# Kernel optimization log

Hardware: AMD Instinct MI355X
Metric: run time of the kernel (lower is better)

Reference implementation:

```python
import jax, jax.numpy as jnp
import numpy as np

TEMPERATURE = 0.1
B, T, D = 8, 1024, 1024
NEG_INF = -1e30

def setup_inputs() -> dict:
    key = jax.random.key(0)
    k1, k2, k3 = jax.random.split(key, 3)
    features = jax.random.normal(k1, (B, T, D), dtype=jnp.float32)
    masks = jax.random.bernoulli(k2, 0.05, (B, 1, T, T)).astype(jnp.float32)
    input_coords_length = jax.random.randint(k3, (B,), T // 2, T - 1)  # int32
    return {"features": features, "masks": masks, "input_coords_length": input_coords_length}


def _sup_con_loss(feat, mask, L):
    # feat: [T, D], mask: [T, T] float, L: scalar int valid length (slice [:L, :L])
    Tn = feat.shape[0]
    dt = feat.dtype
    vr = jnp.arange(Tn) < L                              # valid rows/cols [T]
    valid2d = (vr[:, None] & vr[None, :]).astype(dt)     # [T, T]
    dot = jnp.matmul(feat, feat.T) / TEMPERATURE         # [T, T]
    dot = jnp.where(vr[None, :], dot, NEG_INF)           # exclude padded cols from max
    logits = dot - jax.lax.stop_gradient(jnp.max(dot, axis=-1, keepdims=True))
    logits_mask = (1.0 - jnp.eye(Tn, dtype=dt)) * valid2d  # off-diagonal, in-slice
    exp_logits = jnp.exp(logits) * logits_mask
    m = mask * valid2d
    # negative_mask = 1-mask; entries < 1 zeroed (binary mask -> indicator of mask==0)
    neg = 1.0 - m
    neg = jnp.where(neg < 1.0, 0.0, neg) * valid2d
    # positive_mask = mask with entries > 0 set to 1
    pos = jnp.where(m > 0, 1.0, m)
    neg_denom = jnp.sum(exp_logits * neg, axis=-1, keepdims=True)
    pos_denom = jax.lax.stop_gradient(jnp.sum(exp_logits * pos, axis=-1, keepdims=True))
    log_prob = logits - jnp.log(neg_denom + pos_denom + 1e-6)
    m2 = m * logits_mask
    mean_log_prob_pos = (m2 * log_prob).sum(-1) / (m2.sum(-1) + 1e-6)  # [T]
    # mean over the L valid rows only (matches .mean() on the sliced tensor)
    return -jnp.sum(jnp.where(vr, mean_log_prob_pos, 0.0)) / L.astype(dt)


def _is_valid(mask, L):
    # valid sample iff sliced mask differs from eye(L) with [0,0]=0
    Tn = mask.shape[0]
    vr = jnp.arange(Tn) < L
    valid2d = (vr[:, None] & vr[None, :]).astype(mask.dtype)
    sanity = jnp.eye(Tn, dtype=mask.dtype).at[0, 0].set(0.0) * valid2d
    return jnp.any((mask * valid2d) != sanity)


def reference(features, masks, input_coords_length):
    L = input_coords_length + 1                      # [B]
    mask0 = masks[:, 0]                              # [B, T, T] (num_layers asserted == 1)
    losses = jax.vmap(_sup_con_loss)(features, mask0, L)   # [B]
    valid = jax.vmap(_is_valid)(mask0, L)                  # [B] bool
    vbs = jnp.maximum(jnp.sum(valid.astype(features.dtype)), 1.0)
    return jnp.sum(losses) / vbs
```

## Files before the change

kernel.cpp:

```cpp
#include <hip/hip_runtime.h>
#include <hip/hip_bf16.h>
#include <stdint.h>

#define T_DIM 1024
#define B_DIM 8

typedef __attribute__((ext_vector_type(8))) short short8;
typedef __attribute__((ext_vector_type(4))) float f32x4;

__device__ inline void gll16(const void* g, void* l) {
  __builtin_amdgcn_global_load_lds((__attribute__((address_space(1))) void*)g,
                                   (__attribute__((address_space(3))) void*)l,
                                   16, 0, 0);
}

__global__ __launch_bounds__(256) void convert_kernel(const float* __restrict__ F,
                                                      __hip_bfloat16* __restrict__ Fb) {
  const int t = blockIdx.x * 256 + threadIdx.x;
  const float4 v = ((const float4*)F)[t];
  union { __hip_bfloat16 h[4]; uint64_t u; } p;
  p.h[0] = __float2bfloat16(v.x);
  p.h[1] = __float2bfloat16(v.y);
  p.h[2] = __float2bfloat16(v.z);
  p.h[3] = __float2bfloat16(v.w);
  ((uint64_t*)Fb)[t] = p.u;
}

__global__ __launch_bounds__(512) void fused_kernel(const __hip_bfloat16* __restrict__ Fb,
                                                    const float* __restrict__ M,
                                                    const int* __restrict__ icl,
                                                    float* __restrict__ part) {
  const int b  = blockIdx.z;
  const int rt = blockIdx.y;
  const int ct = blockIdx.x;
  const int L  = icl[b] + 1;
  if (rt * 128 >= L || ct * 128 >= L) return;

  __shared__ char smem[65536];
  __hip_bfloat16* As = (__hip_bfloat16*)smem;
  __hip_bfloat16* Bs = (__hip_bfloat16*)(smem + 32768);
  float* rp = (float*)smem;
  float* rp_m = rp;
  float* rp_d = rp + 512;
  float* rp_s = rp + 1024;
  float* rp_c = rp + 1536;
  float* rp_b = rp + 2048;

  const __hip_bfloat16* F = Fb + ((size_t)b << 20);
  const int tid  = threadIdx.x;
  const int lane = tid & 63;
  const int wave = tid >> 6;
  const int wrow = (wave >> 2) * 64;
  const int wcol = (wave & 3) * 32;
  const int row0 = rt * 128;
  const int col0 = ct * 128;
  const bool diag = (rt == ct);

  const int fr = lane & 15;
  const int q  = lane >> 4;
  const int sl8 = (q ^ ((fr >> 1) & 3)) * 8;

  const int srow = tid >> 2;
  const int sgk  = (((tid & 3) ^ ((tid >> 3) & 3)) * 8);

  f32x4 acc[4][2];
#pragma unroll
  for (int i = 0; i < 4; i++)
#pragma unroll
    for (int j = 0; j < 2; j++) acc[i][j] = (f32x4){0.f, 0.f, 0.f, 0.f};

  for (int k0 = 0; k0 < T_DIM; k0 += 128) {
    __syncthreads();
#pragma unroll
    for (int p = 0; p < 4; p++)
      gll16(F + (size_t)(row0 + srow) * T_DIM + k0 + p * 32 + sgk,
            As + p * 4096 + tid * 8);
    if (!diag) {
#pragma unroll
      for (int p = 0; p < 4; p++)
        gll16(F + (size_t)(col0 + srow) * T_DIM + k0 + p * 32 + sgk,
              Bs + p * 4096 + tid * 8);
    }
    __syncthreads();
#pragma unroll
    for (int kk = 0; kk < 4; kk++) {
      const __hip_bfloat16* Ab = As + kk * 4096;
      const __hip_bfloat16* Bb = diag ? Ab : (Bs + kk * 4096);
      short8 af[4], bfr[2];
#pragma unroll
      for (int t = 0; t < 4; t++)
        af[t] = *(const short8*)(Ab + (wrow + t * 16 + fr) * 32 + sl8);
#pragma unroll
      for (int j = 0; j < 2; j++)
        bfr[j] = *(const short8*)(Bb + (wcol + j * 16 + fr) * 32 + sl8);
#pragma unroll
      for (int ti = 0; ti < 4; ti++)
#pragma unroll
        for (int tj = 0; tj < 2; tj++)
          acc[ti][tj] = __builtin_amdgcn_mfma_f32_16x16x32_bf16(af[ti], bfr[tj], acc[ti][tj], 0, 0, 0);
    }
  }
  __syncthreads();

  const float* Mb = M + ((size_t)b << 20);
  const int gc0 = col0 + wcol + fr;
  const int gc1 = gc0 + 16;
#pragma unroll
  for (int ti = 0; ti < 4; ti++) {
    float mk0[4], mk1[4];
#pragma unroll
    for (int r = 0; r < 4; r++) {
      const int grow = row0 + wrow + ti * 16 + q * 4 + r;
      mk0[r] = (gc0 < L) ? Mb[(size_t)grow * T_DIM + gc0] : 0.f;
      mk1[r] = (gc1 < L) ? Mb[(size_t)grow * T_DIM + gc1] : 0.f;
    }
#pragma unroll
    for (int r = 0; r < 4; r++) {
      const int lrow = wrow + ti * 16 + q * 4 + r;
      const int grow = row0 + lrow;
      const float s0 = (gc0 < L) ? acc[ti][0][r] * 10.0f : -1e30f;
      const float s1 = (gc1 < L) ? acc[ti][1][r] * 10.0f : -1e30f;
      float m = fmaxf(s0, s1);
#pragma unroll
      for (int d = 1; d < 16; d <<= 1) m = fmaxf(m, __shfl_xor(m, d, 64));
      float den = 0.f, msum = 0.f, cnt = 0.f, badf = 0.f;
      if (gc0 < L) {
        if (gc0 != grow) { den += __expf(s0 - m); msum += mk0[r] * s0; cnt += mk0[r]; }
        const float sane = (gc0 == grow && grow != 0) ? 1.f : 0.f;
        badf = fmaxf(badf, (mk0[r] != sane) ? 1.f : 0.f);
      }
      if (gc1 < L) {
        if (gc1 != grow) { den += __expf(s1 - m); msum += mk1[r] * s1; cnt += mk1[r]; }
        const float sane = (gc1 == grow && grow != 0) ? 1.f : 0.f;
        badf = fmaxf(badf, (mk1[r] != sane) ? 1.f : 0.f);
      }
#pragma unroll
      for (int d = 1; d < 16; d <<= 1) {
        den  += __shfl_xor(den, d, 64);
        msum += __shfl_xor(msum, d, 64);
        cnt  += __shfl_xor(cnt, d, 64);
        badf  = fmaxf(badf, __shfl_xor(badf, d, 64));
      }
      if (fr == 0) {
        const int slot = wave & 3;
        rp_m[lrow * 4 + slot] = m;   rp_d[lrow * 4 + slot] = den;
        rp_s[lrow * 4 + slot] = msum; rp_c[lrow * 4 + slot] = cnt;
        rp_b[lrow * 4 + slot] = badf;
      }
    }
  }
  __syncthreads();

  if (tid < 128) {
    float m = -1e30f;
#pragma unroll
    for (int s = 0; s < 4; s++) m = fmaxf(m, rp_m[tid * 4 + s]);
    float den = 0.f, msum = 0.f, cnt = 0.f, badf = 0.f;
#pragma unroll
    for (int s = 0; s < 4; s++) {
      den  += rp_d[tid * 4 + s] * __expf(rp_m[tid * 4 + s] - m);
      msum += rp_s[tid * 4 + s];
      cnt  += rp_c[tid * 4 + s];
      badf  = fmaxf(badf, rp_b[tid * 4 + s]);
    }
    float* p = part + ((((size_t)b * 1024 + row0 + tid) * 8) + ct) * 5;
    p[0] = m; p[1] = den; p[2] = msum; p[3] = cnt; p[4] = badf;
  }
}

__global__ __launch_bounds__(256) void reduce_kernel(const float* __restrict__ part,
                                                     const int* __restrict__ icl,
                                                     float* __restrict__ blk_sum,
                                                     int* __restrict__ blk_bad) {
  const int blk = blockIdx.x;
  const int row = blk * 256 + threadIdx.x;
  const int b = row >> 10;
  const int i = row & 1023;
  const int L = icl[b] + 1;
  float rv = 0.f;
  int bad = 0;
  if (i < L) {
    const float* p = part + (size_t)row * 40;
    const int ns = (L + 127) >> 7;
    float m = -1e30f;
    for (int s = 0; s < ns; s++) m = fmaxf(m, p[s * 5 + 0]);
    float den = 0.f, msum = 0.f, cnt = 0.f, badf = 0.f;
    for (int s = 0; s < ns; s++) {
      den  += p[s * 5 + 1] * __expf(p[s * 5 + 0] - m);
      msum += p[s * 5 + 2];
      cnt  += p[s * 5 + 3];
      badf  = fmaxf(badf, p[s * 5 + 4]);
    }
    const float A = msum - cnt * m;
    const float mlpp = (A - cnt * __logf(den + 1e-6f)) / (cnt + 1e-6f);
    rv = -mlpp / (float)L;
    bad = badf > 0.f ? 1 : 0;
  }
  const int tid  = threadIdx.x;
  const int lane = tid & 63;
  const int wave = tid >> 6;
  for (int o = 32; o > 0; o >>= 1) rv += __shfl_down(rv, o, 64);
  const int wbad = (__ballot(bad) != 0ull) ? 1 : 0;
  __shared__ float sred[4];
  __shared__ int bred[4];
  if (lane == 0) { sred[wave] = rv; bred[wave] = wbad; }
  __syncthreads();
  if (tid == 0) {
    blk_sum[blk] = sred[0] + sred[1] + sred[2] + sred[3];
    blk_bad[blk] = bred[0] | bred[1] | bred[2] | bred[3];
  }
}

__global__ __launch_bounds__(64) void final_kernel(const float* __restrict__ blk_sum,
                                                   const int* __restrict__ blk_bad,
                                                   float* __restrict__ out) {
  const int tid = threadIdx.x;
  float v = (tid < 32) ? blk_sum[tid] : 0.f;
  for (int o = 32; o > 0; o >>= 1) v += __shfl_down(v, o, 64);
  if (tid == 0) {
    int vcount = 0;
    for (int bb = 0; bb < B_DIM; bb++) {
      const int any = blk_bad[bb * 4] | blk_bad[bb * 4 + 1] |
                      blk_bad[bb * 4 + 2] | blk_bad[bb * 4 + 3];
      vcount += any ? 1 : 0;
    }
    out[0] = v / fmaxf((float)vcount, 1.0f);
  }
}

extern "C" void kernel_launch(void* const* d_in, const int* in_sizes, int n_in,
                              void* d_out, int out_size, void* d_ws, size_t ws_size,
                              hipStream_t stream) {
  const float* feat = (const float*)d_in[0];
  const float* mask = (const float*)d_in[1];
  const int*   icl  = (const int*)d_in[2];
  float* out = (float*)d_out;

  char* ws = (char*)d_ws;
  __hip_bfloat16* Fb = (__hip_bfloat16*)ws;
  float* part    = (float*)(ws + (16u << 20));
  float* blk_sum = (float*)(ws + (18u << 20));
  int*   blk_bad = (int*)(ws + (18u << 20) + 512);

  convert_kernel<<<dim3(8192), dim3(256), 0, stream>>>(feat, Fb);
  fused_kernel<<<dim3(8, 8, 8), dim3(512), 0, stream>>>(Fb, mask, icl, part);
  reduce_kernel<<<dim3(32), dim3(256), 0, stream>>>(part, icl, blk_sum, blk_bad);
  final_kernel<<<dim3(1), dim3(64), 0, stream>>>(blk_sum, blk_bad, out);
}
```

Baseline: 134.0 us.

## Shrink GEMM tiles to 64x64 and fold final reduction into last reduce block

The fused GEMM+loss kernel now uses 64x64 output tiles with 256 threads and a 64-wide K step, giving a 16x16x8 grid. The aim is more blocks and higher occupancy, since the 128-tile grid left many CUs idle once tiles past L are skipped. The separate final kernel is removed: reduce blocks publish their partials with release stores and bump an atomic counter, and the last block computes the output. The counter is reset inside the convert kernel. The cost is more redundant global and L2 traffic per tile, twice as many partial slots to reduce, and a dependence on atomic ordering across kernels.

```diff
diff --git a/kernel.cpp b/kernel.cpp
--- a/kernel.cpp
+++ b/kernel.cpp
@@ -15,8 +15,10 @@
 }
 
 __global__ __launch_bounds__(256) void convert_kernel(const float* __restrict__ F,
-                                                      __hip_bfloat16* __restrict__ Fb) {
+                                                      __hip_bfloat16* __restrict__ Fb,
+                                                      int* __restrict__ counter) {
   const int t = blockIdx.x * 256 + threadIdx.x;
+  if (t == 0) __hip_atomic_store(counter, 0, __ATOMIC_RELAXED, __HIP_MEMORY_SCOPE_AGENT);
   const float4 v = ((const float4*)F)[t];
   union { __hip_bfloat16 h[4]; uint64_t u; } p;
   p.h[0] = __float2bfloat16(v.x);
@@ -26,34 +28,34 @@
   ((uint64_t*)Fb)[t] = p.u;
 }
 
-__global__ __launch_bounds__(512) void fused_kernel(const __hip_bfloat16* __restrict__ Fb,
-                                                    const float* __restrict__ M,
-                                                    const int* __restrict__ icl,
-                                                    float* __restrict__ part) {
+__global__ __launch_bounds__(256, 6) void fused_kernel(const __hip_bfloat16* __restrict__ Fb,
+                                                       const float* __restrict__ M,
+                                                       const int* __restrict__ icl,
+                                                       float* __restrict__ part) {
   const int b  = blockIdx.z;
   const int rt = blockIdx.y;
   const int ct = blockIdx.x;
   const int L  = icl[b] + 1;
-  if (rt * 128 >= L || ct * 128 >= L) return;
-
-  __shared__ char smem[65536];
+  if (rt * 64 >= L || ct * 64 >= L) return;
+
+  __shared__ char smem[16384];
   __hip_bfloat16* As = (__hip_bfloat16*)smem;
-  __hip_bfloat16* Bs = (__hip_bfloat16*)(smem + 32768);
+  __hip_bfloat16* Bs = (__hip_bfloat16*)(smem + 8192);
   float* rp = (float*)smem;
   float* rp_m = rp;
-  float* rp_d = rp + 512;
-  float* rp_s = rp + 1024;
-  float* rp_c = rp + 1536;
-  float* rp_b = rp + 2048;
+  float* rp_d = rp + 128;
+  float* rp_s = rp + 256;
+  float* rp_c = rp + 384;
+  float* rp_b = rp + 512;
 
   const __hip_bfloat16* F = Fb + ((size_t)b << 20);
   const int tid  = threadIdx.x;
   const int lane = tid & 63;
   const int wave = tid >> 6;
-  const int wrow = (wave >> 2) * 64;
-  const int wcol = (wave & 3) * 32;
-  const int row0 = rt * 128;
-  const int col0 = ct * 128;
+  const int wrow = (wave >> 1) * 32;
+  const int wcol = (wave & 1) * 32;
+  const int row0 = rt * 64;
+  const int col0 = ct * 64;
   const bool diag = (rt == ct);
 
   const int fr = lane & 15;
@@ -63,38 +65,34 @@
   const int srow = tid >> 2;
   const int sgk  = (((tid & 3) ^ ((tid >> 3) & 3)) * 8);
 
-  f32x4 acc[4][2];
-#pragma unroll
-  for (int i = 0; i < 4; i++)
+  f32x4 acc[2][2];
+#pragma unroll
+  for (int i = 0; i < 2; i++)
 #pragma unroll
     for (int j = 0; j < 2; j++) acc[i][j] = (f32x4){0.f, 0.f, 0.f, 0.f};
 
-  for (int k0 = 0; k0 < T_DIM; k0 += 128) {
+  for (int k0 = 0; k0 < T_DIM; k0 += 64) {
     __syncthreads();
-#pragma unroll
-    for (int p = 0; p < 4; p++)
-      gll16(F + (size_t)(row0 + srow) * T_DIM + k0 + p * 32 + sgk,
-            As + p * 4096 + tid * 8);
+    gll16(F + (size_t)(row0 + srow) * T_DIM + k0 + sgk,      As + tid * 8);
+    gll16(F + (size_t)(row0 + srow) * T_DIM + k0 + 32 + sgk, As + 2048 + tid * 8);
     if (!diag) {
-#pragma unroll
-      for (int p = 0; p < 4; p++)
-        gll16(F + (size_t)(col0 + srow) * T_DIM + k0 + p * 32 + sgk,
-              Bs + p * 4096 + tid * 8);
+      gll16(F + (size_t)(col0 + srow) * T_DIM + k0 + sgk,      Bs + tid * 8);
+      gll16(F + (size_t)(col0 + srow) * T_DIM + k0 + 32 + sgk, Bs + 2048 + tid * 8);
     }
     __syncthreads();
 #pragma unroll
-    for (int kk = 0; kk < 4; kk++) {
-      const __hip_bfloat16* Ab = As + kk * 4096;
-      const __hip_bfloat16* Bb = diag ? Ab : (Bs + kk * 4096);
-      short8 af[4], bfr[2];
-#pragma unroll
-      for (int t = 0; t < 4; t++)
+    for (int kk = 0; kk < 2; kk++) {
+      const __hip_bfloat16* Ab = As + kk * 2048;
+      const __hip_bfloat16* Bb = diag ? Ab : (Bs + kk * 2048);
+      short8 af[2], bfr[2];
+#pragma unroll
+      for (int t = 0; t < 2; t++)
         af[t] = *(const short8*)(Ab + (wrow + t * 16 + fr) * 32 + sl8);
 #pragma unroll
       for (int j = 0; j < 2; j++)
         bfr[j] = *(const short8*)(Bb + (wcol + j * 16 + fr) * 32 + sl8);
 #pragma unroll
-      for (int ti = 0; ti < 4; ti++)
+      for (int ti = 0; ti < 2; ti++)
 #pragma unroll
         for (int tj = 0; tj < 2; tj++)
           acc[ti][tj] = __builtin_amdgcn_mfma_f32_16x16x32_bf16(af[ti], bfr[tj], acc[ti][tj], 0, 0, 0);
@@ -106,7 +104,7 @@
   const int gc0 = col0 + wcol + fr;
   const int gc1 = gc0 + 16;
 #pragma unroll
-  for (int ti = 0; ti < 4; ti++) {
+  for (int ti = 0; ti < 2; ti++) {
     float mk0[4], mk1[4];
 #pragma unroll
     for (int r = 0; r < 4; r++) {
@@ -142,28 +140,24 @@
         badf  = fmaxf(badf, __shfl_xor(badf, d, 64));
       }
       if (fr == 0) {
-        const int slot = wave & 3;
-        rp_m[lrow * 4 + slot] = m;   rp_d[lrow * 4 + slot] = den;
-        rp_s[lrow * 4 + slot] = msum; rp_c[lrow * 4 + slot] = cnt;
-        rp_b[lrow * 4 + slot] = badf;
+        const int slot = wave & 1;
+        rp_m[lrow * 2 + slot] = m;    rp_d[lrow * 2 + slot] = den;
+        rp_s[lrow * 2 + slot] = msum; rp_c[lrow * 2 + slot] = cnt;
+        rp_b[lrow * 2 + slot] = badf;
       }
     }
   }
   __syncthreads();
 
-  if (tid < 128) {
-    float m = -1e30f;
-#pragma unroll
-    for (int s = 0; s < 4; s++) m = fmaxf(m, rp_m[tid * 4 + s]);
-    float den = 0.f, msum = 0.f, cnt = 0.f, badf = 0.f;
-#pragma unroll
-    for (int s = 0; s < 4; s++) {
-      den  += rp_d[tid * 4 + s] * __expf(rp_m[tid * 4 + s] - m);
-      msum += rp_s[tid * 4 + s];
-      cnt  += rp_c[tid * 4 + s];
-      badf  = fmaxf(badf, rp_b[tid * 4 + s]);
-    }
-    float* p = part + ((((size_t)b * 1024 + row0 + tid) * 8) + ct) * 5;
+  if (tid < 64) {
+    const float m0 = rp_m[tid * 2 + 0], m1 = rp_m[tid * 2 + 1];
+    const float m = fmaxf(m0, m1);
+    const float den = rp_d[tid * 2 + 0] * __expf(m0 - m) +
+                      rp_d[tid * 2 + 1] * __expf(m1 - m);
+    const float msum = rp_s[tid * 2 + 0] + rp_s[tid * 2 + 1];
+    const float cnt  = rp_c[tid * 2 + 0] + rp_c[tid * 2 + 1];
+    const float badf = fmaxf(rp_b[tid * 2 + 0], rp_b[tid * 2 + 1]);
+    float* p = part + ((((size_t)b * 1024 + row0 + tid) * 16) + ct) * 5;
     p[0] = m; p[1] = den; p[2] = msum; p[3] = cnt; p[4] = badf;
   }
 }
@@ -171,7 +165,9 @@
 __global__ __launch_bounds__(256) void reduce_kernel(const float* __restrict__ part,
                                                      const int* __restrict__ icl,
                                                      float* __restrict__ blk_sum,
-                                                     int* __restrict__ blk_bad) {
+                                                     int* __restrict__ blk_bad,
+                                                     int* __restrict__ counter,
+                                                     float* __restrict__ out) {
   const int blk = blockIdx.x;
   const int row = blk * 256 + threadIdx.x;
   const int b = row >> 10;
@@ -180,8 +176,8 @@
   float rv = 0.f;
   int bad = 0;
   if (i < L) {
-    const float* p = part + (size_t)row * 40;
-    const int ns = (L + 127) >> 7;
+    const float* p = part + (size_t)row * 80;
+    const int ns = (L + 63) >> 6;
     float m = -1e30f;
     for (int s = 0; s < ns; s++) m = fmaxf(m, p[s * 5 + 0]);
     float den = 0.f, msum = 0.f, cnt = 0.f, badf = 0.f;
@@ -206,25 +202,24 @@
   if (lane == 0) { sred[wave] = rv; bred[wave] = wbad; }
   __syncthreads();
   if (tid == 0) {
-    blk_sum[blk] = sred[0] + sred[1] + sred[2] + sred[3];
-    blk_bad[blk] = bred[0] | bred[1] | bred[2] | bred[3];
-  }
-}
-
-__global__ __launch_bounds__(64) void final_kernel(const float* __restrict__ blk_sum,
-                                                   const int* __restrict__ blk_bad,
-                                                   float* __restrict__ out) {
-  const int tid = threadIdx.x;
-  float v = (tid < 32) ? blk_sum[tid] : 0.f;
-  for (int o = 32; o > 0; o >>= 1) v += __shfl_down(v, o, 64);
-  if (tid == 0) {
-    int vcount = 0;
-    for (int bb = 0; bb < B_DIM; bb++) {
-      const int any = blk_bad[bb * 4] | blk_bad[bb * 4 + 1] |
-                      blk_bad[bb * 4 + 2] | blk_bad[bb * 4 + 3];
-      vcount += any ? 1 : 0;
-    }
-    out[0] = v / fmaxf((float)vcount, 1.0f);
+    const float bs = sred[0] + sred[1] + sred[2] + sred[3];
+    const int bb = bred[0] | bred[1] | bred[2] | bred[3];
+    __hip_atomic_store(&blk_sum[blk], bs, __ATOMIC_RELEASE, __HIP_MEMORY_SCOPE_AGENT);
+    __hip_atomic_store(&blk_bad[blk], bb, __ATOMIC_RELEASE, __HIP_MEMORY_SCOPE_AGENT);
+    const int old = __hip_atomic_fetch_add(counter, 1, __ATOMIC_ACQ_REL, __HIP_MEMORY_SCOPE_AGENT);
+    if (old == 31) {
+      float total = 0.f;
+      for (int k = 0; k < 32; k++)
+        total += __hip_atomic_load(&blk_sum[k], __ATOMIC_ACQUIRE, __HIP_MEMORY_SCOPE_AGENT);
+      int vcount = 0;
+      for (int bb2 = 0; bb2 < B_DIM; bb2++) {
+        int any = 0;
+        for (int k = 0; k < 4; k++)
+          any |= __hip_atomic_load(&blk_bad[bb2 * 4 + k], __ATOMIC_ACQUIRE, __HIP_MEMORY_SCOPE_AGENT);
+        vcount += any ? 1 : 0;
+      }
+      out[0] = total / fmaxf((float)vcount, 1.0f);
+    }
   }
 }
 
@@ -239,11 +234,11 @@
   char* ws = (char*)d_ws;
   __hip_bfloat16* Fb = (__hip_bfloat16*)ws;
   float* part    = (float*)(ws + (16u << 20));
-  float* blk_sum = (float*)(ws + (18u << 20));
-  int*   blk_bad = (int*)(ws + (18u << 20) + 512);
-
-  convert_kernel<<<dim3(8192), dim3(256), 0, stream>>>(feat, Fb);
-  fused_kernel<<<dim3(8, 8, 8), dim3(512), 0, stream>>>(Fb, mask, icl, part);
-  reduce_kernel<<<dim3(32), dim3(256), 0, stream>>>(part, icl, blk_sum, blk_bad);
-  final_kernel<<<dim3(1), dim3(64), 0, stream>>>(blk_sum, blk_bad, out);
-}
+  float* blk_sum = (float*)(ws + (19u << 20));
+  int*   blk_bad = (int*)(ws + (19u << 20) + 512);
+  int*   counter = (int*)(ws + (19u << 20) + 1024);
+
+  convert_kernel<<<dim3(8192), dim3(256), 0, stream>>>(feat, Fb, counter);
+  fused_kernel<<<dim3(16, 16, 8), dim3(256), 0, stream>>>(Fb, mask, icl, part);
+  reduce_kernel<<<dim3(32), dim3(256), 0, stream>>>(part, icl, blk_sum, blk_bad, counter, out);
+}
```

Result: slower. 156.1 us (+16.5%).
